# Kernel optimization log

Hardware: AMD Instinct MI355X
Metric: run time of the kernel (lower is better)

## Reference

```python
import jax, jax.numpy as jnp
import numpy as np

EPS = 1e-6

def _l2normalize(x, axis=1):
    # matches torch: x / sqrt(sum(x^2) + eps)
    norm = jnp.sqrt(jnp.sum(x * x, axis=axis, keepdims=True) + EPS)
    return x / norm


def setup_inputs() -> dict:
    key = jax.random.key(0)
    k1, k2, k3 = jax.random.split(key, 3)
    B, C, H, W = 8, 64, 48, 48
    x = jax.random.normal(k1, (B, C, H, W), dtype=jnp.float32)
    v = jax.random.normal(k2, (B, C, H, W), dtype=jnp.float32)
    pos = jax.random.normal(k3, (B, C, H, W), dtype=jnp.float32)
    # learned scalar parameters (init values from the torch module)
    gamma = jnp.float32(0.0)
    beta_gamma = jnp.float32(10.0)
    sum_gamma0 = jnp.float32(0.0)
    sum_gamma1 = jnp.float32(0.0)
    return {"x": x, "v": v, "pos": pos, "gamma": gamma,
            "beta_gamma": beta_gamma, "sum_gamma0": sum_gamma0,
            "sum_gamma1": sum_gamma1}


def reference(x, v, pos, gamma, beta_gamma, sum_gamma0, sum_gamma1):
    B, C, H, W = x.shape
    N = H * W
    # q and k are computed identically in the original module; compute once.
    q = _l2normalize(x + gamma * pos, axis=1)          # [B, C, H, W]
    qf = q.reshape(B, C, N)                             # [B, C, N]
    vf = v.reshape(B, v.shape[1], N)                    # [B, Cv, N]
    # scores[b, n, m] = <q[:, n], k[:, m]>; learned temperature beta_gamma
    scores = jnp.einsum('bcn,bcm->bnm', qf, qf) * beta_gamma  # [B, N, N]
    beta = jax.nn.softmax(scores, axis=-1)              # [B, N, N]
    # o = v @ beta^T  => o[b, c, n] = sum_m v[b, c, m] * beta[b, n, m]
    o = jnp.einsum('bcm,bnm->bcn', vf, beta).reshape(B, vf.shape[1], H, W)
    e0 = jnp.exp(sum_gamma0)
    e1 = jnp.exp(sum_gamma1)
    tot = e0 + e1
    out = (e0 / tot) * o + (e1 / tot) * v
    return out, beta.reshape(B, N, H, W)
```

## Files before the change

kernel.cpp:

```cpp
#include <hip/hip_runtime.h>
#include <hip/hip_bf16.h>

#define B_  8
#define C_  64
#define N_  2304
#define TS  64
#define NT_ (N_ / TS)
#define LDP 72

typedef __attribute__((ext_vector_type(8))) short  short8;
typedef __attribute__((ext_vector_type(4))) float  floatx4;

struct Hdr { int f32mode; float gamma, bg, cmax, w0, w1; };

__device__ __forceinline__ float bf2f(unsigned short u) {
  return __uint_as_float(((unsigned int)u) << 16);
}
__device__ __forceinline__ unsigned short f2bf(float f) {
  unsigned int x = __float_as_uint(f);
  x += 0x7fff + ((x >> 16) & 1);
  return (unsigned short)(x >> 16);
}

__global__ void detect_k(const void* g, const void* bgp, const void* s0,
                         const void* s1, Hdr* h) {
  if (threadIdx.x == 0 && blockIdx.x == 0) {
    int f32 = (((const unsigned short*)bgp)[0] == 0) ? 1 : 0;
    float gamma, bg, sg0, sg1;
    if (f32) {
      gamma = ((const float*)g)[0];  bg  = ((const float*)bgp)[0];
      sg0   = ((const float*)s0)[0]; sg1 = ((const float*)s1)[0];
    } else {
      gamma = bf2f(((const unsigned short*)g)[0]);
      bg    = bf2f(((const unsigned short*)bgp)[0]);
      sg0   = bf2f(((const unsigned short*)s0)[0]);
      sg1   = bf2f(((const unsigned short*)s1)[0]);
    }
    float e0 = __expf(sg0), e1 = __expf(sg1);
    h->f32mode = f32;
    h->gamma = gamma;
    h->bg = bg;
    h->cmax = fabsf(bg);
    h->w0 = e0 / (e0 + e1);
    h->w1 = e1 / (e0 + e1);
  }
}

__global__ __launch_bounds__(256)
void prep_q(const void* __restrict__ xv, const void* __restrict__ posv,
            const void* __restrict__ vv_raw, const Hdr* __restrict__ h,
            unsigned short* __restrict__ qT, unsigned short* __restrict__ vb) {
  int t = blockIdx.x * 256 + threadIdx.x;
  int b = t / N_;
  int n = t - b * N_;
  const bool f32 = h->f32mode;
  float gamma = h->gamma;
  float vals[C_];
  float s = 0.f;
  if (f32) {
    const float* xp = (const float*)xv  + (size_t)b * C_ * N_ + n;
    const float* pp = (const float*)posv + (size_t)b * C_ * N_ + n;
#pragma unroll
    for (int c = 0; c < C_; ++c) {
      float val = xp[(size_t)c * N_] + gamma * pp[(size_t)c * N_];
      vals[c] = val;  s += val * val;
    }
  } else {
    const unsigned short* xp = (const unsigned short*)xv  + (size_t)b * C_ * N_ + n;
    const unsigned short* pp = (const unsigned short*)posv + (size_t)b * C_ * N_ + n;
#pragma unroll
    for (int c = 0; c < C_; ++c) {
      float val = bf2f(xp[(size_t)c * N_]) + gamma * bf2f(pp[(size_t)c * N_]);
      vals[c] = val;  s += val * val;
    }
  }
  float inv = rsqrtf(s + 1e-6f);
  unsigned int* qrow = reinterpret_cast<unsigned int*>(qT + (size_t)t * C_);
#pragma unroll
  for (int c = 0; c < C_; c += 2) {
    qrow[c >> 1] = (unsigned int)f2bf(vals[c] * inv)
                 | ((unsigned int)f2bf(vals[c + 1] * inv) << 16);
  }
  const int NU32 = (B_ * C_ * N_) / 2;
  const int TC   = (B_ * N_);
  unsigned int* vb32 = reinterpret_cast<unsigned int*>(vb);
  if (f32) {
    const float* vf = (const float*)vv_raw;
    for (int i = t; i < NU32; i += TC) {
      float f0 = vf[2 * i], f1 = vf[2 * i + 1];
      vb32[i] = (unsigned int)f2bf(f0) | ((unsigned int)f2bf(f1) << 16);
    }
  } else {
    const unsigned int* v32 = (const unsigned int*)vv_raw;
    for (int i = t; i < NU32; i += TC) vb32[i] = v32[i];
  }
}

__global__ __launch_bounds__(256)
void pass1_rowsum(const unsigned short* __restrict__ qT,
                  const Hdr* __restrict__ h,
                  float* __restrict__ rowsum) {
  __shared__ unsigned short qm[TS * LDP];
  int b  = blockIdx.x / NT_;
  int n0 = (blockIdx.x - b * NT_) * TS;
  int tid  = threadIdx.x;
  int wave = tid >> 6;
  int lane = tid & 63;
  int quad = lane >> 4;
  int l15  = lane & 15;
  float bg = h->bg, cmax = h->cmax;
  const unsigned short* abase =
      qT + ((size_t)(b * N_ + n0 + 16 * wave + l15)) * C_ + quad * 8;
  short8 a0 = *reinterpret_cast<const short8*>(abase);
  short8 a1 = *reinterpret_cast<const short8*>(abase + 32);
  float acc[4] = {0.f, 0.f, 0.f, 0.f};
  for (int mt = 0; mt < NT_; ++mt) {
    int m0 = mt * TS;
    __syncthreads();
#pragma unroll
    for (int k = 0; k < 2; ++k) {
      int chunk = tid + 256 * k;
      int row = chunk >> 3;
      int col = (chunk & 7) * 8;
      short8 vv = *reinterpret_cast<const short8*>(
          qT + ((size_t)(b * N_ + m0 + row)) * C_ + col);
      *reinterpret_cast<short8*>(&qm[row * LDP + col]) = vv;
    }
    __syncthreads();
#pragma unroll
    for (int j = 0; j < 4; ++j) {
      short8 b0 = *reinterpret_cast<const short8*>(&qm[(j * 16 + l15) * LDP + quad * 8]);
      short8 b1 = *reinterpret_cast<const short8*>(&qm[(j * 16 + l15) * LDP + 32 + quad * 8]);
      floatx4 d = {0.f, 0.f, 0.f, 0.f};
      d = __builtin_amdgcn_mfma_f32_16x16x32_bf16(a0, b0, d, 0, 0, 0);
      d = __builtin_amdgcn_mfma_f32_16x16x32_bf16(a1, b1, d, 0, 0, 0);
#pragma unroll
      for (int r = 0; r < 4; ++r)
        acc[r] += __expf(d[r] * bg - cmax);
    }
  }
#pragma unroll
  for (int r = 0; r < 4; ++r) {
    float vv = acc[r];
    vv += __shfl_xor(vv, 1);
    vv += __shfl_xor(vv, 2);
    vv += __shfl_xor(vv, 4);
    vv += __shfl_xor(vv, 8);
    acc[r] = vv;
  }
  if (l15 == 0) {
#pragma unroll
    for (int r = 0; r < 4; ++r)
      rowsum[(size_t)b * N_ + n0 + 16 * wave + quad * 4 + r] = acc[r];
  }
}

__global__ __launch_bounds__(256)
void pass2_attn(const unsigned short* __restrict__ qT,
                const unsigned short* __restrict__ vb,
                const void* __restrict__ vraw,
                const Hdr* __restrict__ h,
                const float* __restrict__ rowsum,
                void* __restrict__ dout) {
  __shared__ unsigned short qm[TS * LDP];
  __shared__ unsigned short vt[TS * LDP];
  __shared__ unsigned short pt[TS * LDP];
  int b  = blockIdx.x / NT_;
  int n0 = (blockIdx.x - b * NT_) * TS;
  int tid  = threadIdx.x;
  int wave = tid >> 6;
  int lane = tid & 63;
  int quad = lane >> 4;
  int l15  = lane & 15;
  const bool f32 = h->f32mode;
  float bg = h->bg, cmax = h->cmax, w0 = h->w0, w1 = h->w1;
  unsigned short* out16  = (unsigned short*)dout;
  unsigned short* beta16 = out16 + (size_t)B_ * C_ * N_;
  float* out32  = (float*)dout;
  float* beta32 = out32 + (size_t)B_ * C_ * N_;

  const unsigned short* abase =
      qT + ((size_t)(b * N_ + n0 + 16 * wave + l15)) * C_ + quad * 8;
  short8 a0 = *reinterpret_cast<const short8*>(abase);
  short8 a1 = *reinterpret_cast<const short8*>(abase + 32);
  float inv[4];
#pragma unroll
  for (int r = 0; r < 4; ++r)
    inv[r] = 1.f / rowsum[(size_t)b * N_ + n0 + 16 * wave + quad * 4 + r];
  floatx4 oacc[4] = {{0.f,0.f,0.f,0.f},{0.f,0.f,0.f,0.f},
                     {0.f,0.f,0.f,0.f},{0.f,0.f,0.f,0.f}};
  for (int mt = 0; mt < NT_; ++mt) {
    int m0 = mt * TS;
    __syncthreads();
#pragma unroll
    for (int k = 0; k < 2; ++k) {
      int chunk = tid + 256 * k;
      int row = chunk >> 3;
      int col = (chunk & 7) * 8;
      short8 qv = *reinterpret_cast<const short8*>(
          qT + ((size_t)(b * N_ + m0 + row)) * C_ + col);
      *reinterpret_cast<short8*>(&qm[row * LDP + col]) = qv;
      short8 vv = *reinterpret_cast<const short8*>(
          vb + ((size_t)(b * C_ + row)) * N_ + m0 + col);
      *reinterpret_cast<short8*>(&vt[row * LDP + col]) = vv;
    }
    __syncthreads();
#pragma unroll
    for (int j = 0; j < 4; ++j) {
      short8 b0 = *reinterpret_cast<const short8*>(&qm[(j * 16 + l15) * LDP + quad * 8]);
      short8 b1 = *reinterpret_cast<const short8*>(&qm[(j * 16 + l15) * LDP + 32 + quad * 8]);
      floatx4 d = {0.f, 0.f, 0.f, 0.f};
      d = __builtin_amdgcn_mfma_f32_16x16x32_bf16(a0, b0, d, 0, 0, 0);
      d = __builtin_amdgcn_mfma_f32_16x16x32_bf16(a1, b1, d, 0, 0, 0);
#pragma unroll
      for (int r = 0; r < 4; ++r) {
        float p = __expf(d[r] * bg - cmax) * inv[r];
        pt[(16 * wave + quad * 4 + r) * LDP + j * 16 + l15] = f2bf(p);
        if (f32) {
          beta32[((size_t)(b * N_ + n0 + 16 * wave + quad * 4 + r)) * N_
                 + m0 + j * 16 + l15] = p;
        }
      }
    }
    __syncthreads();
    if (!f32) {
#pragma unroll
      for (int k = 0; k < 2; ++k) {
        int chunk = tid + 256 * k;
        int row = chunk >> 3;
        int col = (chunk & 7) * 8;
        short8 pv = *reinterpret_cast<const short8*>(&pt[row * LDP + col]);
        *reinterpret_cast<short8*>(
            beta16 + ((size_t)(b * N_ + n0 + row)) * N_ + m0 + col) = pv;
      }
    }
    short8 av0 = *reinterpret_cast<const short8*>(&vt[(16 * wave + l15) * LDP + quad * 8]);
    short8 av1 = *reinterpret_cast<const short8*>(&vt[(16 * wave + l15) * LDP + 32 + quad * 8]);
#pragma unroll
    for (int j = 0; j < 4; ++j) {
      short8 bp0 = *reinterpret_cast<const short8*>(&pt[(j * 16 + l15) * LDP + quad * 8]);
      short8 bp1 = *reinterpret_cast<const short8*>(&pt[(j * 16 + l15) * LDP + 32 + quad * 8]);
      oacc[j] = __builtin_amdgcn_mfma_f32_16x16x32_bf16(av0, bp0, oacc[j], 0, 0, 0);
      oacc[j] = __builtin_amdgcn_mfma_f32_16x16x32_bf16(av1, bp1, oacc[j], 0, 0, 0);
    }
  }
#pragma unroll
  for (int j = 0; j < 4; ++j) {
#pragma unroll
    for (int r = 0; r < 4; ++r) {
      int c = 16 * wave + quad * 4 + r;
      int n = n0 + 16 * j + l15;
      size_t idx = ((size_t)(b * C_ + c)) * N_ + n;
      if (f32) {
        float vvf = ((const float*)vraw)[idx];
        out32[idx] = w0 * oacc[j][r] + w1 * vvf;
      } else {
        float vvf = bf2f(((const unsigned short*)vraw)[idx]);
        out16[idx] = f2bf(w0 * oacc[j][r] + w1 * vvf);
      }
    }
  }
}

extern "C" void kernel_launch(void* const* d_in, const int* in_sizes, int n_in,
                              void* d_out, int out_size, void* d_ws, size_t ws_size,
                              hipStream_t stream) {
  const void* x     = d_in[0];
  const void* v     = d_in[1];
  const void* pos   = d_in[2];
  const void* gamma = d_in[3];
  const void* bg    = d_in[4];
  const void* sg0   = d_in[5];
  const void* sg1   = d_in[6];

  char* ws = (char*)d_ws;
  Hdr* hdr = (Hdr*)ws;
  unsigned short* qT = (unsigned short*)(ws + 256);
  unsigned short* vb = (unsigned short*)(ws + 256 + (size_t)B_ * N_ * C_ * 2);
  float* rowsum = (float*)(ws + 256 + (size_t)B_ * N_ * C_ * 4);

  detect_k<<<dim3(1), dim3(64), 0, stream>>>(gamma, bg, sg0, sg1, hdr);
  prep_q<<<dim3((B_ * N_) / 256), dim3(256), 0, stream>>>(x, pos, v, hdr, qT, vb);
  pass1_rowsum<<<dim3(B_ * NT_), dim3(256), 0, stream>>>(qT, hdr, rowsum);
  pass2_attn<<<dim3(B_ * NT_), dim3(256), 0, stream>>>(qT, vb, v, hdr, rowsum, d_out);
}
```

Baseline: 273.3 us.

## Fuse rowsum and attention passes into one kernel holding a 16-row score strip in LDS

Replaces the two-pass scheme, which computed QK^T twice, with a single kernel per 16 query rows. The kernel keeps all unnormalised exponentials for the strip in shared memory (about 74KB), reduces the row sums across waves, then runs PV from LDS and writes the normalised beta with vectorised stores. This removes the duplicated score GEMM and exp work and one launch. In exchange, B fragments are read straight from global memory without LDS tiling, the large LDS footprint limits occupancy, and beta is rounded to bf16 before normalisation even in fp32 mode.

```diff
diff --git a/kernel.cpp b/kernel.cpp
--- a/kernel.cpp
+++ b/kernel.cpp
@@ -1,12 +1,10 @@
 #include <hip/hip_runtime.h>
-#include <hip/hip_bf16.h>
-
-#define B_  8
-#define C_  64
-#define N_  2304
-#define TS  64
-#define NT_ (N_ / TS)
-#define LDP 72
+
+#define B_   8
+#define C_   64
+#define N_   2304
+#define NBLK 144
+#define LDN  2312
 
 typedef __attribute__((ext_vector_type(8))) short  short8;
 typedef __attribute__((ext_vector_type(4))) float  floatx4;
@@ -58,7 +56,7 @@
   float vals[C_];
   float s = 0.f;
   if (f32) {
-    const float* xp = (const float*)xv  + (size_t)b * C_ * N_ + n;
+    const float* xp = (const float*)xv   + (size_t)b * C_ * N_ + n;
     const float* pp = (const float*)posv + (size_t)b * C_ * N_ + n;
 #pragma unroll
     for (int c = 0; c < C_; ++c) {
@@ -66,7 +64,7 @@
       vals[c] = val;  s += val * val;
     }
   } else {
-    const unsigned short* xp = (const unsigned short*)xv  + (size_t)b * C_ * N_ + n;
+    const unsigned short* xp = (const unsigned short*)xv   + (size_t)b * C_ * N_ + n;
     const unsigned short* pp = (const unsigned short*)posv + (size_t)b * C_ * N_ + n;
 #pragma unroll
     for (int c = 0; c < C_; ++c) {
@@ -92,51 +90,53 @@
     }
   } else {
     const unsigned int* v32 = (const unsigned int*)vv_raw;
-    for (int i = t; i < NU32; i += TC) vb32[i] = v32[i];
+    for (int i = t; i < TC * 0 + NU32; i += TC) vb32[i] = v32[i];
   }
 }
 
 __global__ __launch_bounds__(256)
-void pass1_rowsum(const unsigned short* __restrict__ qT,
-                  const Hdr* __restrict__ h,
-                  float* __restrict__ rowsum) {
-  __shared__ unsigned short qm[TS * LDP];
-  int b  = blockIdx.x / NT_;
-  int n0 = (blockIdx.x - b * NT_) * TS;
+void fused_attn(const unsigned short* __restrict__ qT,
+                const unsigned short* __restrict__ vb,
+                const void* __restrict__ vraw,
+                const Hdr* __restrict__ h,
+                void* __restrict__ dout) {
+  __shared__ unsigned short pnum[16 * LDN];
+  __shared__ float rs[16][4];
+  __shared__ float invs[16];
+  int b  = blockIdx.x / NBLK;
+  int nb = blockIdx.x - b * NBLK;
+  int n0 = nb * 16;
   int tid  = threadIdx.x;
   int wave = tid >> 6;
   int lane = tid & 63;
   int quad = lane >> 4;
   int l15  = lane & 15;
-  float bg = h->bg, cmax = h->cmax;
+  const bool f32m = h->f32mode;
+  float bg = h->bg, cmax = h->cmax, w0 = h->w0, w1 = h->w1;
+
   const unsigned short* abase =
-      qT + ((size_t)(b * N_ + n0 + 16 * wave + l15)) * C_ + quad * 8;
+      qT + ((size_t)(b * N_ + n0 + l15)) * C_ + quad * 8;
   short8 a0 = *reinterpret_cast<const short8*>(abase);
   short8 a1 = *reinterpret_cast<const short8*>(abase + 32);
   float acc[4] = {0.f, 0.f, 0.f, 0.f};
-  for (int mt = 0; mt < NT_; ++mt) {
-    int m0 = mt * TS;
-    __syncthreads();
-#pragma unroll
-    for (int k = 0; k < 2; ++k) {
-      int chunk = tid + 256 * k;
-      int row = chunk >> 3;
-      int col = (chunk & 7) * 8;
-      short8 vv = *reinterpret_cast<const short8*>(
-          qT + ((size_t)(b * N_ + m0 + row)) * C_ + col);
-      *reinterpret_cast<short8*>(&qm[row * LDP + col]) = vv;
-    }
-    __syncthreads();
-#pragma unroll
-    for (int j = 0; j < 4; ++j) {
-      short8 b0 = *reinterpret_cast<const short8*>(&qm[(j * 16 + l15) * LDP + quad * 8]);
-      short8 b1 = *reinterpret_cast<const short8*>(&qm[(j * 16 + l15) * LDP + 32 + quad * 8]);
+  for (int mt = wave; mt < 36; mt += 4) {
+    int m0 = mt * 64;
+#pragma unroll
+    for (int sub = 0; sub < 4; ++sub) {
+      int mb = m0 + sub * 16;
+      const unsigned short* bbase =
+          qT + ((size_t)(b * N_ + mb + l15)) * C_ + quad * 8;
+      short8 b0 = *reinterpret_cast<const short8*>(bbase);
+      short8 b1 = *reinterpret_cast<const short8*>(bbase + 32);
       floatx4 d = {0.f, 0.f, 0.f, 0.f};
       d = __builtin_amdgcn_mfma_f32_16x16x32_bf16(a0, b0, d, 0, 0, 0);
       d = __builtin_amdgcn_mfma_f32_16x16x32_bf16(a1, b1, d, 0, 0, 0);
 #pragma unroll
-      for (int r = 0; r < 4; ++r)
-        acc[r] += __expf(d[r] * bg - cmax);
+      for (int r = 0; r < 4; ++r) {
+        float e = __expf(d[r] * bg - cmax);
+        acc[r] += e;
+        pnum[(quad * 4 + r) * LDN + mb + l15] = f2bf(e);
+      }
     }
   }
 #pragma unroll
@@ -146,118 +146,74 @@
     vv += __shfl_xor(vv, 2);
     vv += __shfl_xor(vv, 4);
     vv += __shfl_xor(vv, 8);
-    acc[r] = vv;
-  }
-  if (l15 == 0) {
-#pragma unroll
-    for (int r = 0; r < 4; ++r)
-      rowsum[(size_t)b * N_ + n0 + 16 * wave + quad * 4 + r] = acc[r];
-  }
-}
-
-__global__ __launch_bounds__(256)
-void pass2_attn(const unsigned short* __restrict__ qT,
-                const unsigned short* __restrict__ vb,
-                const void* __restrict__ vraw,
-                const Hdr* __restrict__ h,
-                const float* __restrict__ rowsum,
-                void* __restrict__ dout) {
-  __shared__ unsigned short qm[TS * LDP];
-  __shared__ unsigned short vt[TS * LDP];
-  __shared__ unsigned short pt[TS * LDP];
-  int b  = blockIdx.x / NT_;
-  int n0 = (blockIdx.x - b * NT_) * TS;
-  int tid  = threadIdx.x;
-  int wave = tid >> 6;
-  int lane = tid & 63;
-  int quad = lane >> 4;
-  int l15  = lane & 15;
-  const bool f32 = h->f32mode;
-  float bg = h->bg, cmax = h->cmax, w0 = h->w0, w1 = h->w1;
+    if (l15 == 0) rs[quad * 4 + r][wave] = vv;
+  }
+  __syncthreads();
+  if (tid < 16)
+    invs[tid] = 1.f / (rs[tid][0] + rs[tid][1] + rs[tid][2] + rs[tid][3]);
+  __syncthreads();
+
+  floatx4 o = {0.f, 0.f, 0.f, 0.f};
+  const unsigned short* vrow =
+      vb + ((size_t)(b * C_ + 16 * wave + l15)) * N_;
+  const unsigned short* prow = pnum + l15 * LDN;
+#pragma unroll 4
+  for (int m0 = 0; m0 < N_; m0 += 32) {
+    short8 av = *reinterpret_cast<const short8*>(vrow + m0 + quad * 8);
+    short8 bp = *reinterpret_cast<const short8*>(prow + m0 + quad * 8);
+    o = __builtin_amdgcn_mfma_f32_16x16x32_bf16(av, bp, o, 0, 0, 0);
+  }
+  float invn = invs[l15];
+
+  float* out32  = (float*)dout;
+  float* beta32 = out32 + (size_t)B_ * C_ * N_;
   unsigned short* out16  = (unsigned short*)dout;
   unsigned short* beta16 = out16 + (size_t)B_ * C_ * N_;
-  float* out32  = (float*)dout;
-  float* beta32 = out32 + (size_t)B_ * C_ * N_;
-
-  const unsigned short* abase =
-      qT + ((size_t)(b * N_ + n0 + 16 * wave + l15)) * C_ + quad * 8;
-  short8 a0 = *reinterpret_cast<const short8*>(abase);
-  short8 a1 = *reinterpret_cast<const short8*>(abase + 32);
-  float inv[4];
-#pragma unroll
-  for (int r = 0; r < 4; ++r)
-    inv[r] = 1.f / rowsum[(size_t)b * N_ + n0 + 16 * wave + quad * 4 + r];
-  floatx4 oacc[4] = {{0.f,0.f,0.f,0.f},{0.f,0.f,0.f,0.f},
-                     {0.f,0.f,0.f,0.f},{0.f,0.f,0.f,0.f}};
-  for (int mt = 0; mt < NT_; ++mt) {
-    int m0 = mt * TS;
-    __syncthreads();
-#pragma unroll
-    for (int k = 0; k < 2; ++k) {
-      int chunk = tid + 256 * k;
-      int row = chunk >> 3;
-      int col = (chunk & 7) * 8;
-      short8 qv = *reinterpret_cast<const short8*>(
-          qT + ((size_t)(b * N_ + m0 + row)) * C_ + col);
-      *reinterpret_cast<short8*>(&qm[row * LDP + col]) = qv;
-      short8 vv = *reinterpret_cast<const short8*>(
-          vb + ((size_t)(b * C_ + row)) * N_ + m0 + col);
-      *reinterpret_cast<short8*>(&vt[row * LDP + col]) = vv;
-    }
-    __syncthreads();
-#pragma unroll
-    for (int j = 0; j < 4; ++j) {
-      short8 b0 = *reinterpret_cast<const short8*>(&qm[(j * 16 + l15) * LDP + quad * 8]);
-      short8 b1 = *reinterpret_cast<const short8*>(&qm[(j * 16 + l15) * LDP + 32 + quad * 8]);
-      floatx4 d = {0.f, 0.f, 0.f, 0.f};
-      d = __builtin_amdgcn_mfma_f32_16x16x32_bf16(a0, b0, d, 0, 0, 0);
-      d = __builtin_amdgcn_mfma_f32_16x16x32_bf16(a1, b1, d, 0, 0, 0);
-#pragma unroll
-      for (int r = 0; r < 4; ++r) {
-        float p = __expf(d[r] * bg - cmax) * inv[r];
-        pt[(16 * wave + quad * 4 + r) * LDP + j * 16 + l15] = f2bf(p);
-        if (f32) {
-          beta32[((size_t)(b * N_ + n0 + 16 * wave + quad * 4 + r)) * N_
-                 + m0 + j * 16 + l15] = p;
-        }
+
+  for (int k = 0; k < 9; ++k) {
+    int c   = k * 256 + tid;
+    int row = c / 144;
+    int ms  = (c - row * 144) * 16;
+    float iv = invs[row];
+    const unsigned short* pp = pnum + row * LDN + ms;
+    short8 p0 = *reinterpret_cast<const short8*>(pp);
+    short8 p1 = *reinterpret_cast<const short8*>(pp + 8);
+    float vals[16];
+#pragma unroll
+    for (int i = 0; i < 8; ++i) {
+      vals[i]     = bf2f((unsigned short)p0[i]) * iv;
+      vals[8 + i] = bf2f((unsigned short)p1[i]) * iv;
+    }
+    size_t base = ((size_t)(b * N_ + n0 + row)) * N_ + ms;
+    if (f32m) {
+      floatx4* dst = reinterpret_cast<floatx4*>(beta32 + base);
+#pragma unroll
+      for (int q = 0; q < 4; ++q) {
+        floatx4 wv = {vals[4*q], vals[4*q+1], vals[4*q+2], vals[4*q+3]};
+        dst[q] = wv;
       }
-    }
-    __syncthreads();
-    if (!f32) {
-#pragma unroll
-      for (int k = 0; k < 2; ++k) {
-        int chunk = tid + 256 * k;
-        int row = chunk >> 3;
-        int col = (chunk & 7) * 8;
-        short8 pv = *reinterpret_cast<const short8*>(&pt[row * LDP + col]);
-        *reinterpret_cast<short8*>(
-            beta16 + ((size_t)(b * N_ + n0 + row)) * N_ + m0 + col) = pv;
+    } else {
+      short8 o0, o1;
+#pragma unroll
+      for (int i = 0; i < 8; ++i) {
+        o0[i] = (short)f2bf(vals[i]);
+        o1[i] = (short)f2bf(vals[8 + i]);
       }
-    }
-    short8 av0 = *reinterpret_cast<const short8*>(&vt[(16 * wave + l15) * LDP + quad * 8]);
-    short8 av1 = *reinterpret_cast<const short8*>(&vt[(16 * wave + l15) * LDP + 32 + quad * 8]);
-#pragma unroll
-    for (int j = 0; j < 4; ++j) {
-      short8 bp0 = *reinterpret_cast<const short8*>(&pt[(j * 16 + l15) * LDP + quad * 8]);
-      short8 bp1 = *reinterpret_cast<const short8*>(&pt[(j * 16 + l15) * LDP + 32 + quad * 8]);
-      oacc[j] = __builtin_amdgcn_mfma_f32_16x16x32_bf16(av0, bp0, oacc[j], 0, 0, 0);
-      oacc[j] = __builtin_amdgcn_mfma_f32_16x16x32_bf16(av1, bp1, oacc[j], 0, 0, 0);
-    }
-  }
-#pragma unroll
-  for (int j = 0; j < 4; ++j) {
-#pragma unroll
-    for (int r = 0; r < 4; ++r) {
-      int c = 16 * wave + quad * 4 + r;
-      int n = n0 + 16 * j + l15;
-      size_t idx = ((size_t)(b * C_ + c)) * N_ + n;
-      if (f32) {
-        float vvf = ((const float*)vraw)[idx];
-        out32[idx] = w0 * oacc[j][r] + w1 * vvf;
-      } else {
-        float vvf = bf2f(((const unsigned short*)vraw)[idx]);
-        out16[idx] = f2bf(w0 * oacc[j][r] + w1 * vvf);
-      }
+      short8* dst = reinterpret_cast<short8*>(beta16 + base);
+      dst[0] = o0;  dst[1] = o1;
+    }
+  }
+
+#pragma unroll
+  for (int r = 0; r < 4; ++r) {
+    int cc = 16 * wave + quad * 4 + r;
+    int nn = n0 + l15;
+    size_t idx = ((size_t)(b * C_ + cc)) * N_ + nn;
+    float ov = o[r] * invn;
+    if (f32m) {
+      out32[idx] = w0 * ov + w1 * ((const float*)vraw)[idx];
+    } else {
+      out16[idx] = f2bf(w0 * ov + w1 * bf2f(((const unsigned short*)vraw)[idx]));
     }
   }
 }
@@ -277,10 +233,8 @@
   Hdr* hdr = (Hdr*)ws;
   unsigned short* qT = (unsigned short*)(ws + 256);
   unsigned short* vb = (unsigned short*)(ws + 256 + (size_t)B_ * N_ * C_ * 2);
-  float* rowsum = (float*)(ws + 256 + (size_t)B_ * N_ * C_ * 4);
 
   detect_k<<<dim3(1), dim3(64), 0, stream>>>(gamma, bg, sg0, sg1, hdr);
   prep_q<<<dim3((B_ * N_) / 256), dim3(256), 0, stream>>>(x, pos, v, hdr, qT, vb);
-  pass1_rowsum<<<dim3(B_ * NT_), dim3(256), 0, stream>>>(qT, hdr, rowsum);
-  pass2_attn<<<dim3(B_ * NT_), dim3(256), 0, stream>>>(qT, vb, v, hdr, rowsum, d_out);
-}
+  fused_attn<<<dim3(B_ * NBLK), dim3(256), 0, stream>>>(qT, vb, v, hdr, d_out);
+}
```

New measurement: 310.8 us. 13.7% more time.
